# Kernel tuning notes

Measured on AMD Instinct MI355X. Metric: run time of the kernel, lower is better.

## Reference

```python
import jax, jax.numpy as jnp
import numpy as np

NS, NC, T, NB = 32, 16, 64, 512
NSC = NS + NC


def setup_inputs() -> dict:
    key = jax.random.key(0)
    k1, k2, k3, k4, k5 = jax.random.split(key, 5)
    # SPD cost matrices so Quu is invertible (as assumed by the LQR math)
    L = jax.random.normal(k1, (NB, T, NSC, NSC), jnp.float32) * 0.1
    Q = L @ jnp.swapaxes(L, -1, -2) + jnp.eye(NSC, dtype=jnp.float32)
    p = jax.random.normal(k2, (NB, T, NSC), jnp.float32)
    x_init = jax.random.normal(k3, (NB, NS), jnp.float32)
    # stable-ish LTI dynamics
    A = 0.9 * jnp.eye(NS, dtype=jnp.float32) + 0.01 * jax.random.normal(k4, (NS, NS), jnp.float32)
    B = 0.1 * jax.random.normal(k5, (NS, NC), jnp.float32)
    dt = jnp.float32(0.1)
    return {"x_init": x_init, "Q": Q, "p": p, "A": A, "B": B, "dt": dt}


def _lqr(x_init, Q, p, A, B):
    ns, nc = A.shape[0], B.shape[1]
    nb, Th = Q.shape[0], Q.shape[1]
    dtype = Q.dtype

    # --- nominal rollout with zero control: x_{t+1} = A x_t ---
    def roll(x, _):
        return x @ A.T, x
    _, cx = jax.lax.scan(roll, x_init, None, length=Th)   # [T,B,ns] states x_0..x_{T-1}
    cu = jnp.zeros((Th, nb, nc), dtype)                    # current_u = 0
    xu = jnp.concatenate([cx, cu], -1)                     # [T,B,nsc]

    Qs = jnp.swapaxes(Q, 0, 1)                             # [T,B,nsc,nsc]
    ps = jnp.swapaxes(p, 0, 1)                             # [T,B,nsc]
    p_new = jnp.einsum('tbij,tbj->tbi', Qs, xu) + ps       # [T,B,nsc]

    F = jnp.concatenate([A, B], axis=1)                    # [ns, nsc]

    # --- backward Riccati recursion (V=v=0 at t=T-1 makes Qt=Q[T-1]) ---
    def bwd(carry, inp):
        V, v = carry                                       # [B,ns,ns], [B,ns]
        Qt_in, qt_in = inp
        Qt = Qt_in + jnp.einsum('si,bst,tj->bij', F, V, F)
        qt = qt_in + v @ F                                 # F^T v
        Qxx, Qxu = Qt[:, :ns, :ns], Qt[:, :ns, ns:]
        Qux, Quu = Qt[:, ns:, :ns], Qt[:, ns:, ns:]
        qx, qu = qt[:, :ns], qt[:, ns:]
        Quu_inv = jnp.linalg.pinv(Quu)
        Kt = -Quu_inv @ Qux                                # [B,nc,ns]
        kt = -jnp.einsum('bij,bj->bi', Quu_inv, qu)        # [B,nc]
        KtT = jnp.swapaxes(Kt, -1, -2)
        Vn = Qxx + Qxu @ Kt + KtT @ Qux + KtT @ Quu @ Kt
        vn = (qx + jnp.einsum('bij,bj->bi', Qxu, kt)
              + jnp.einsum('bij,bj->bi', KtT, qu)
              + jnp.einsum('bij,bj->bi', KtT @ Quu, kt))
        return (Vn, vn), (Kt, kt)

    V0 = jnp.zeros((nb, ns, ns), dtype)
    v0 = jnp.zeros((nb, ns), dtype)
    _, (Ks, ks) = jax.lax.scan(bwd, (V0, v0), (Qs, p_new), reverse=True)

    # --- forward rollout with feedback policy ---
    def fwd(carry, inp):
        xt, cost = carry
        Kt, kt, cxt, cut, Qt, pt = inp
        dut = jnp.einsum('bij,bj->bi', Kt, xt - cxt) + kt
        ut = dut + cut
        xut = jnp.concatenate([xt, ut], -1)
        cost = cost + 0.5 * jnp.einsum('bi,bij,bj->b', xut, Qt, xut) + (xut * pt).sum(-1)
        xn = xt @ A.T + ut @ B.T
        return (xn, cost), (xt, ut)

    (_, cost), (xs, us) = jax.lax.scan(
        fwd, (x_init, jnp.zeros(nb, dtype)), (Ks, ks, cx, cu, Qs, ps))
    x = jnp.swapaxes(xs, 0, 1)   # [B,T,ns]  (states x_0..x_{T-1}, matching x[...,:-1,:])
    u = jnp.swapaxes(us, 0, 1)   # [B,T,nc]
    return x, u, cost


def reference(x_init, Q, p, A, B, dt):
    # dt only matters for nonlinear relinearization; with constant LTI (A,B) it is unused.
    return _lqr(x_init, Q, p, A, B)
```

## Files before the change

kernel.cpp:

```cpp
#include <hip/hip_runtime.h>


#define NSd 32
#define NCd 16
#define Td 64
#define NBd 512
#define NSCd 48
#define SQS 52
#define TP 40

typedef __bf16 bf16x8 __attribute__((ext_vector_type(8)));
typedef __bf16 bf16x4 __attribute__((ext_vector_type(4)));
typedef float f32x4 __attribute__((ext_vector_type(4)));

#define MFMA16(a, b, c) __builtin_amdgcn_mfma_f32_16x16x32_bf16(a, b, c, 0, 0, 0)

#define XOFF ((size_t)0)
#define UOFF ((size_t)NBd * Td * NSd)
#define COFF (UOFF + (size_t)NBd * Td * NCd)

__device__ __forceinline__ float rdl(float v, int l) {
  return __uint_as_float(__builtin_amdgcn_readlane(__float_as_uint(v), l));
}

__device__ __forceinline__ void bar_lgkm() {
  asm volatile("s_waitcnt lgkmcnt(0)\n\ts_barrier" ::: "memory");
}

union LdsU {
  struct {
    __bf16 FTh[48][TP], FTl[48][TP];
    __bf16 Vh[32][TP], Vl[32][TP];
    __bf16 WTh[48][TP], WTl[48][TP];
    __bf16 Xh[32][TP], Xl[32][TP];
    __bf16 KTh[32][TP], KTl[32][TP];
    float Quu[16][17];
    float qt[48];
    float vv[32];
    float kt[16];
  } bw;
  struct {
    float K2T[2][16 * 36];
    float kv2[2][16];
    float d[32];
    float xs[32];
    float uu[16];
  } fw;
};

#define SQSTORE(i, v)                            \
  do {                                           \
    int _r = (i) / 12, _c = (i) - _r * 12;       \
    *(float4*)&sQ[_r * SQS + _c * 4] = (v);      \
  } while (0)

__global__ __launch_bounds__(256, 2) void lqr_kernel(
    const float* __restrict__ x_init, const float* __restrict__ Qg,
    const float* __restrict__ pg, const float* __restrict__ Ag,
    const float* __restrict__ Bg, float* __restrict__ out,
    float* __restrict__ wsK, float* __restrict__ wskv) {
  const int b = blockIdx.x;
  const int tid = threadIdx.x;
  const int w = tid >> 6;
  const int lane = tid & 63;
  const int fn = lane & 15;
  const int quad = lane >> 4;
  const int k0 = quad * 8;

  __shared__ __attribute__((aligned(16))) float sQ[48 * SQS];
  __shared__ __attribute__((aligned(16))) float scx[Td][NSd];
  __shared__ __attribute__((aligned(16))) float sFf[NSd][SQS];
  __shared__ __attribute__((aligned(16))) LdsU U;
  __shared__ float scostp[4];

  for (int idx = tid; idx < 1536; idx += 256) {
    int i = idx / 48, j = idx - i * 48;
    sFf[i][j] = (j < 32) ? Ag[i * 32 + j] : Bg[i * 16 + (j - 32)];
  }
  for (int idx = tid; idx < 1536; idx += 256) {
    int a = idx >> 5, k = idx & 31;
    float f = (a < 32) ? Ag[k * 32 + a] : Bg[k * 16 + (a - 32)];
    __bf16 h = (__bf16)f;
    U.bw.FTh[a][k] = h;
    U.bw.FTl[a][k] = (__bf16)(f - (float)h);
  }
  for (int idx = tid; idx < 1024; idx += 256) {
    int r = idx >> 5, c = idx & 31;
    __bf16 z = (__bf16)0.f;
    U.bw.Vh[r][c] = z; U.bw.Vl[r][c] = z;
    U.bw.Xh[r][c] = z; U.bw.Xl[r][c] = z;
    U.bw.KTh[r][c] = z; U.bw.KTl[r][c] = z;
  }
  if (tid < 32) {
    scx[0][tid] = x_init[b * 32 + tid];
    U.bw.vv[tid] = 0.f;
  }
  {
    const float4* src = (const float4*)(Qg + ((size_t)b * Td + 63) * 2304);
    float4 v0 = src[tid];
    float4 v1 = src[tid + 256];
    SQSTORE(tid, v0);
    SQSTORE(tid + 256, v1);
    if (tid < 64) {
      float4 v2 = src[tid + 512];
      SQSTORE(tid + 512, v2);
    }
  }
  float ppf = 0.f;
  if (w == 3 && lane < 48) ppf = pg[((size_t)b * Td + 63) * 48 + lane];
  __syncthreads();

  if (w == 0) {
    for (int t2 = 0; t2 < Td - 1; ++t2) {
      if (lane < 32) {
        float acc = 0.f;
#pragma unroll
        for (int j = 0; j < 32; j += 4) {
          float4 a4 = *(const float4*)&sFf[lane][j];
          acc += a4.x * scx[t2][j] + a4.y * scx[t2][j + 1] +
                 a4.z * scx[t2][j + 2] + a4.w * scx[t2][j + 3];
        }
        scx[t2 + 1][lane] = acc;
      }
    }
  }
  __syncthreads();

  float cAcc = 0.f;
  float dAcc = 0.f;

  for (int t = Td - 1; t >= 0; --t) {
    const int sw = 3 - (t & 1);
    float4 pf0, pf1, pf2;
    float ppfn;
    if (t > 0) {
      const float4* src = (const float4*)(Qg + ((size_t)b * Td + (t - 1)) * 2304);
      pf0 = src[tid];
      pf1 = src[tid + 256];
      if (tid < 64) pf2 = src[tid + 512];
      if (w == 3 && lane < 48) ppfn = pg[((size_t)b * Td + t - 1) * 48 + lane];
    }
    if (w < 3) {
      const int I = w;
      bf16x8 aH = *(const bf16x8*)&U.bw.FTh[16 * I + fn][k0];
      bf16x8 aL = *(const bf16x8*)&U.bw.FTl[16 * I + fn][k0];
#pragma unroll
      for (int J = 0; J < 2; ++J) {
        bf16x8 bH = *(const bf16x8*)&U.bw.Vh[16 * J + fn][k0];
        bf16x8 bL = *(const bf16x8*)&U.bw.Vl[16 * J + fn][k0];
        f32x4 acc = {0.f, 0.f, 0.f, 0.f};
        acc = MFMA16(aL, bH, acc);
        acc = MFMA16(aH, bL, acc);
        acc = MFMA16(aH, bH, acc);
#pragma unroll
        for (int r = 0; r < 4; ++r) {
          float v = acc[r];
          __bf16 h = (__bf16)v;
          U.bw.WTh[16 * I + 4 * quad + r][16 * J + fn] = h;
          U.bw.WTl[16 * I + 4 * quad + r][16 * J + fn] = (__bf16)(v - (float)h);
        }
      }
    } else if (lane < 48) {
      float acc1 = ppf;
#pragma unroll
      for (int k = 0; k < 32; ++k) acc1 += sQ[k * SQS + lane] * scx[t][k];
      if (lane < 32) cAcc += 0.5f * scx[t][lane] * (acc1 + ppf);
      float acc = acc1;
#pragma unroll
      for (int k = 0; k < 32; ++k) acc += U.bw.vv[k] * sFf[k][lane];
      U.bw.qt[lane] = acc;
    }
    bar_lgkm();

    f32x4 accQ = {0.f, 0.f, 0.f, 0.f};
    if (w < 2) {
      const int I = w;
      bf16x8 aH = *(const bf16x8*)&U.bw.WTh[16 * I + fn][k0];
      bf16x8 aL = *(const bf16x8*)&U.bw.WTl[16 * I + fn][k0];
      {
        bf16x8 bH = *(const bf16x8*)&U.bw.FTh[16 * I + fn][k0];
        bf16x8 bL = *(const bf16x8*)&U.bw.FTl[16 * I + fn][k0];
#pragma unroll
        for (int r = 0; r < 4; ++r)
          accQ[r] = sQ[(16 * I + 4 * quad + r) * SQS + 16 * I + fn];
        accQ = MFMA16(aL, bH, accQ);
        accQ = MFMA16(aH, bL, accQ);
        accQ = MFMA16(aH, bH, accQ);
      }
      {
        bf16x8 bH = *(const bf16x8*)&U.bw.FTh[32 + fn][k0];
        bf16x8 bL = *(const bf16x8*)&U.bw.FTl[32 + fn][k0];
        f32x4 acc;
#pragma unroll
        for (int r = 0; r < 4; ++r)
          acc[r] = sQ[(16 * I + 4 * quad + r) * SQS + 32 + fn];
        acc = MFMA16(aL, bH, acc);
        acc = MFMA16(aH, bL, acc);
        acc = MFMA16(aH, bH, acc);
#pragma unroll
        for (int r = 0; r < 4; ++r) {
          float v = acc[r];
          __bf16 h = (__bf16)v;
          U.bw.Xh[16 * I + 4 * quad + r][fn] = h;
          U.bw.Xl[16 * I + 4 * quad + r][fn] = (__bf16)(v - (float)h);
        }
      }
    } else if (w == 2) {
      bf16x8 aH = *(const bf16x8*)&U.bw.WTh[fn][k0];
      bf16x8 aL = *(const bf16x8*)&U.bw.WTl[fn][k0];
      bf16x8 bH = *(const bf16x8*)&U.bw.FTh[16 + fn][k0];
      bf16x8 bL = *(const bf16x8*)&U.bw.FTl[16 + fn][k0];
#pragma unroll
      for (int r = 0; r < 4; ++r)
        accQ[r] = sQ[(4 * quad + r) * SQS + 16 + fn];
      accQ = MFMA16(aL, bH, accQ);
      accQ = MFMA16(aH, bL, accQ);
      accQ = MFMA16(aH, bH, accQ);
    } else {
      bf16x8 aH = *(const bf16x8*)&U.bw.WTh[32 + fn][k0];
      bf16x8 aL = *(const bf16x8*)&U.bw.WTl[32 + fn][k0];
      bf16x8 bH = *(const bf16x8*)&U.bw.FTh[32 + fn][k0];
      bf16x8 bL = *(const bf16x8*)&U.bw.FTl[32 + fn][k0];
      f32x4 acc;
#pragma unroll
      for (int r = 0; r < 4; ++r)
        acc[r] = sQ[(32 + 4 * quad + r) * SQS + 32 + fn];
      acc = MFMA16(aL, bH, acc);
      acc = MFMA16(aH, bL, acc);
      acc = MFMA16(aH, bH, acc);
#pragma unroll
      for (int r = 0; r < 4; ++r) U.bw.Quu[4 * quad + r][fn] = acc[r];
    }
    bar_lgkm();

    if (t > 0) {
      SQSTORE(tid, pf0);
      SQSTORE(tid + 256, pf1);
      if (tid < 64) SQSTORE(tid + 512, pf2);
      if (w == 3 && lane < 48) ppf = ppfn;
    }

    if (w == sw) {
      float rhs[16];
      if (lane < 32) {
        bf16x8 xh0 = *(const bf16x8*)&U.bw.Xh[lane][0];
        bf16x8 xh1 = *(const bf16x8*)&U.bw.Xh[lane][8];
        bf16x8 xl0 = *(const bf16x8*)&U.bw.Xl[lane][0];
        bf16x8 xl1 = *(const bf16x8*)&U.bw.Xl[lane][8];
#pragma unroll
        for (int i = 0; i < 8; ++i) {
          rhs[i] = (float)xh0[i] + (float)xl0[i];
          rhs[8 + i] = (float)xh1[i] + (float)xl1[i];
        }
      } else {
#pragma unroll
        for (int i = 0; i < 16; ++i) rhs[i] = U.bw.qt[32 + i];
      }
      float quu[16];
#pragma unroll
      for (int i = 0; i < 16; ++i) quu[i] = U.bw.Quu[i][fn];
#pragma unroll
      for (int r = 0; r < 15; ++r) {
        float inv = __builtin_amdgcn_rcpf(rdl(quu[r], r));
#pragma unroll
        for (int i = r + 1; i < 16; ++i) {
          float m = rdl(quu[i], r) * inv;
          rhs[i] -= m * rhs[r];
          quu[i] -= m * quu[r];
        }
      }
      float xx[16];
#pragma unroll
      for (int r = 15; r >= 0; --r) {
        float s = rhs[r];
#pragma unroll
        for (int c = r + 1; c < 16; ++c) s -= rdl(quu[r], c) * xx[c];
        xx[r] = s * __builtin_amdgcn_rcpf(rdl(quu[r], r));
      }
      if (lane < 32) {
        bf16x8 h0, l0, h1, l1;
#pragma unroll
        for (int u = 0; u < 8; ++u) {
          float kv = -xx[u];
          __bf16 hh = (__bf16)kv;
          h0[u] = hh; l0[u] = (__bf16)(kv - (float)hh);
          float kv2 = -xx[8 + u];
          __bf16 hh2 = (__bf16)kv2;
          h1[u] = hh2; l1[u] = (__bf16)(kv2 - (float)hh2);
        }
        *(bf16x8*)&U.bw.KTh[lane][0] = h0;
        *(bf16x8*)&U.bw.KTh[lane][8] = h1;
        *(bf16x8*)&U.bw.KTl[lane][0] = l0;
        *(bf16x8*)&U.bw.KTl[lane][8] = l1;
        float4* dst = (float4*)(wsK + (((size_t)b * Td + t) * 32 + lane) * 16);
        float4 v0 = {-xx[0], -xx[1], -xx[2], -xx[3]};
        float4 v1 = {-xx[4], -xx[5], -xx[6], -xx[7]};
        float4 v2 = {-xx[8], -xx[9], -xx[10], -xx[11]};
        float4 v3 = {-xx[12], -xx[13], -xx[14], -xx[15]};
        dst[0] = v0; dst[1] = v1; dst[2] = v2; dst[3] = v3;
      } else if (lane == 32) {
#pragma unroll
        for (int u = 0; u < 16; ++u) U.bw.kt[u] = -xx[u];
        float4* dst = (float4*)(wskv + ((size_t)b * Td + t) * 16);
        float4 v0 = {-xx[0], -xx[1], -xx[2], -xx[3]};
        float4 v1 = {-xx[4], -xx[5], -xx[6], -xx[7]};
        float4 v2 = {-xx[8], -xx[9], -xx[10], -xx[11]};
        float4 v3 = {-xx[12], -xx[13], -xx[14], -xx[15]};
        dst[0] = v0; dst[1] = v1; dst[2] = v2; dst[3] = v3;
        float s = 0.f;
#pragma unroll
        for (int i = 0; i < 16; ++i) s += U.bw.qt[32 + i] * xx[i];
        dAcc -= 0.5f * s;
      }
      if (sw == 3) {
        float acc = 0.f;
        bf16x8 xh0, xh1, xl0, xl1;
        if (lane < 32) {
          xh0 = *(const bf16x8*)&U.bw.Xh[lane][0];
          xh1 = *(const bf16x8*)&U.bw.Xh[lane][8];
          xl0 = *(const bf16x8*)&U.bw.Xl[lane][0];
          xl1 = *(const bf16x8*)&U.bw.Xl[lane][8];
          acc = U.bw.qt[lane];
        }
#pragma unroll
        for (int u = 0; u < 8; ++u) {
          float kt0 = -rdl(xx[u], 32);
          float kt1 = -rdl(xx[8 + u], 32);
          if (lane < 32) {
            acc += ((float)xh0[u] + (float)xl0[u]) * kt0;
            acc += ((float)xh1[u] + (float)xl1[u]) * kt1;
          }
        }
        if (lane < 32) U.bw.vv[lane] = acc;
      }
    }
    bar_lgkm();

    if (w == 0) {
      bf16x8 aH = *(const bf16x8*)&U.bw.Xh[fn][k0];
      bf16x8 aL = *(const bf16x8*)&U.bw.Xl[fn][k0];
      bf16x8 bH = *(const bf16x8*)&U.bw.KTh[fn][k0];
      bf16x8 bL = *(const bf16x8*)&U.bw.KTl[fn][k0];
      accQ = MFMA16(aL, bH, accQ);
      accQ = MFMA16(aH, bL, accQ);
      accQ = MFMA16(aH, bH, accQ);
#pragma unroll
      for (int r = 0; r < 4; ++r) {
        float v = accQ[r];
        __bf16 h = (__bf16)v;
        U.bw.Vh[4 * quad + r][fn] = h;
        U.bw.Vl[4 * quad + r][fn] = (__bf16)(v - (float)h);
      }
    } else if (w == 1) {
      bf16x8 aH = *(const bf16x8*)&U.bw.Xh[16 + fn][k0];
      bf16x8 aL = *(const bf16x8*)&U.bw.Xl[16 + fn][k0];
      bf16x8 bH = *(const bf16x8*)&U.bw.KTh[16 + fn][k0];
      bf16x8 bL = *(const bf16x8*)&U.bw.KTl[16 + fn][k0];
      accQ = MFMA16(aL, bH, accQ);
      accQ = MFMA16(aH, bL, accQ);
      accQ = MFMA16(aH, bH, accQ);
#pragma unroll
      for (int r = 0; r < 4; ++r) {
        float v = accQ[r];
        __bf16 h = (__bf16)v;
        U.bw.Vh[16 + 4 * quad + r][16 + fn] = h;
        U.bw.Vl[16 + 4 * quad + r][16 + fn] = (__bf16)(v - (float)h);
      }
    } else if (w == 2) {
      bf16x8 aH = *(const bf16x8*)&U.bw.Xh[fn][k0];
      bf16x8 aL = *(const bf16x8*)&U.bw.Xl[fn][k0];
      bf16x8 bH = *(const bf16x8*)&U.bw.KTh[16 + fn][k0];
      bf16x8 bL = *(const bf16x8*)&U.bw.KTl[16 + fn][k0];
      accQ = MFMA16(aL, bH, accQ);
      accQ = MFMA16(aH, bL, accQ);
      accQ = MFMA16(aH, bH, accQ);
      bf16x4 th, tl;
#pragma unroll
      for (int r = 0; r < 4; ++r) {
        float v = accQ[r];
        __bf16 h = (__bf16)v;
        __bf16 l = (__bf16)(v - (float)h);
        U.bw.Vh[4 * quad + r][16 + fn] = h;
        U.bw.Vl[4 * quad + r][16 + fn] = l;
        th[r] = h; tl[r] = l;
      }
      *(bf16x4*)&U.bw.Vh[16 + fn][4 * quad] = th;
      *(bf16x4*)&U.bw.Vl[16 + fn][4 * quad] = tl;
    } else if (sw == 2) {
      if (lane < 32) {
        bf16x8 xh0 = *(const bf16x8*)&U.bw.Xh[lane][0];
        bf16x8 xh1 = *(const bf16x8*)&U.bw.Xh[lane][8];
        bf16x8 xl0 = *(const bf16x8*)&U.bw.Xl[lane][0];
        bf16x8 xl1 = *(const bf16x8*)&U.bw.Xl[lane][8];
        float acc = U.bw.qt[lane];
#pragma unroll
        for (int u = 0; u < 8; ++u) {
          acc += ((float)xh0[u] + (float)xl0[u]) * U.bw.kt[u];
          acc += ((float)xh1[u] + (float)xl1[u]) * U.bw.kt[8 + u];
        }
        U.bw.vv[lane] = acc;
      }
    }
    bar_lgkm();
  }

  if (w == 3) {
    float rv = (lane < 32) ? cAcc : 0.f;
    rv += __shfl_down(rv, 32);
    rv += __shfl_down(rv, 16);
    rv += __shfl_down(rv, 8);
    rv += __shfl_down(rv, 4);
    rv += __shfl_down(rv, 2);
    rv += __shfl_down(rv, 1);
    if (lane == 0) scostp[0] = rv;
  }
  if (lane == 32 && w >= 2) scostp[w - 1] = dAcc;
  __syncthreads();

  if (w == 0) {
    {
      const float4* src = (const float4*)(wsK + ((size_t)b * Td) * 512);
      float4 ka = src[lane * 2], kb = src[lane * 2 + 1];
      int jj = lane >> 1, ib = (lane & 1) * 8;
      float* kt2 = U.fw.K2T[0];
      kt2[(ib + 0) * 36 + jj] = ka.x; kt2[(ib + 1) * 36 + jj] = ka.y;
      kt2[(ib + 2) * 36 + jj] = ka.z; kt2[(ib + 3) * 36 + jj] = ka.w;
      kt2[(ib + 4) * 36 + jj] = kb.x; kt2[(ib + 5) * 36 + jj] = kb.y;
      kt2[(ib + 6) * 36 + jj] = kb.z; kt2[(ib + 7) * 36 + jj] = kb.w;
      if (lane < 16) U.fw.kv2[0][lane] = wskv[(size_t)b * Td * 16 + lane];
    }
    float xr = (lane < 32) ? scx[0][lane] : 0.f;
    for (int t = 0; t < Td; ++t) {
      const int cur = t & 1, nxt = cur ^ 1;
      float4 pa, pb;
      float pk;
      if (t < Td - 1) {
        const float4* src = (const float4*)(wsK + ((size_t)b * Td + t + 1) * 512);
        pa = src[lane * 2];
        pb = src[lane * 2 + 1];
        if (lane < 16) pk = wskv[((size_t)b * Td + t + 1) * 16 + lane];
      }
      if (lane < 32) {
        U.fw.d[lane] = xr - scx[t][lane];
        U.fw.xs[lane] = xr;
        out[XOFF + ((size_t)b * Td + t) * 32 + lane] = xr;
      }
      if (lane < 16) {
        float uv = U.fw.kv2[cur][lane];
        const float* kr = &U.fw.K2T[cur][lane * 36];
#pragma unroll
        for (int j4 = 0; j4 < 8; ++j4) {
          float4 kk = *(const float4*)&kr[j4 * 4];
          float4 dd = *(const float4*)&U.fw.d[j4 * 4];
          uv += kk.x * dd.x + kk.y * dd.y + kk.z * dd.z + kk.w * dd.w;
        }
        U.fw.uu[lane] = uv;
        out[UOFF + ((size_t)b * Td + t) * 16 + lane] = uv;
      }
      if (lane < 32) {
        float acc = 0.f;
#pragma unroll
        for (int j4 = 0; j4 < 8; ++j4) {
          float4 ff = *(const float4*)&sFf[lane][j4 * 4];
          float4 xv = *(const float4*)&U.fw.xs[j4 * 4];
          acc += ff.x * xv.x + ff.y * xv.y + ff.z * xv.z + ff.w * xv.w;
        }
#pragma unroll
        for (int j4 = 0; j4 < 4; ++j4) {
          float4 ff = *(const float4*)&sFf[lane][32 + j4 * 4];
          float4 uv = *(const float4*)&U.fw.uu[j4 * 4];
          acc += ff.x * uv.x + ff.y * uv.y + ff.z * uv.z + ff.w * uv.w;
        }
        xr = acc;
      }
      if (t < Td - 1) {
        int jj = lane >> 1, ib = (lane & 1) * 8;
        float* kt2 = U.fw.K2T[nxt];
        kt2[(ib + 0) * 36 + jj] = pa.x; kt2[(ib + 1) * 36 + jj] = pa.y;
        kt2[(ib + 2) * 36 + jj] = pa.z; kt2[(ib + 3) * 36 + jj] = pa.w;
        kt2[(ib + 4) * 36 + jj] = pb.x; kt2[(ib + 5) * 36 + jj] = pb.y;
        kt2[(ib + 6) * 36 + jj] = pb.z; kt2[(ib + 7) * 36 + jj] = pb.w;
        if (lane < 16) U.fw.kv2[nxt][lane] = pk;
      }
    }
    if (lane == 0) out[COFF + b] = scostp[0] + scostp[1] + scostp[2];
  }
}

extern "C" void kernel_launch(void* const* d_in, const int* in_sizes, int n_in,
                              void* d_out, int out_size, void* d_ws, size_t ws_size,
                              hipStream_t stream) {
  const float* x_init = (const float*)d_in[0];
  const float* Qg = (const float*)d_in[1];
  const float* pg = (const float*)d_in[2];
  const float* Ag = (const float*)d_in[3];
  const float* Bg = (const float*)d_in[4];
  float* out = (float*)d_out;
  float* wsK = (float*)d_ws;
  float* wskv = wsK + (size_t)NBd * Td * NSd * NCd;
  lqr_kernel<<<NBd, 256, 0, stream>>>(x_init, Qg, pg, Ag, Bg, out, wsK, wskv);
}
```

Before: 663.4 us.

## Restructure backward Riccati step into two barrier phases with fixed wave roles

Each backward step is reorganized so waves 0-2 compute W=F^T V and then the Qt blocks (Qxx pieces, Qxu, Quu) before the first barrier. A single fixed wave 3 then does the Quu solve, the v update and all three V-block MFMAs, instead of alternating solver waves with extra barriers. This removes two of the four block barriers per timestep and the alternating-wave bookkeeping. The cost is serializing more MFMA work onto wave 3 and some extra LDS for the Qd staging. The Q prefetch is also spread over three waves instead of four.

Measured after the change: 636.2 us. 1.04x faster.

```diff
diff --git a/kernel.cpp b/kernel.cpp
--- a/kernel.cpp
+++ b/kernel.cpp
@@ -35,9 +35,9 @@
     __bf16 Xh[32][TP], Xl[32][TP];
     __bf16 KTh[32][TP], KTl[32][TP];
     float Quu[16][17];
+    float Qd[3][16][17];
     float qt[48];
     float vv[32];
-    float kt[16];
   } bw;
   struct {
     float K2T[2][16 * 36];
@@ -130,16 +130,19 @@
   float dAcc = 0.f;
 
   for (int t = Td - 1; t >= 0; --t) {
-    const int sw = 3 - (t & 1);
     float4 pf0, pf1, pf2;
     float ppfn;
     if (t > 0) {
-      const float4* src = (const float4*)(Qg + ((size_t)b * Td + (t - 1)) * 2304);
-      pf0 = src[tid];
-      pf1 = src[tid + 256];
-      if (tid < 64) pf2 = src[tid + 512];
-      if (w == 3 && lane < 48) ppfn = pg[((size_t)b * Td + t - 1) * 48 + lane];
-    }
+      if (w < 3) {
+        const float4* src = (const float4*)(Qg + ((size_t)b * Td + (t - 1)) * 2304);
+        pf0 = src[tid];
+        pf1 = src[tid + 192];
+        pf2 = src[tid + 384];
+      } else if (lane < 48) {
+        ppfn = pg[((size_t)b * Td + t - 1) * 48 + lane];
+      }
+    }
+
     if (w < 3) {
       const int I = w;
       bf16x8 aH = *(const bf16x8*)&U.bw.FTh[16 * I + fn][k0];
@@ -160,6 +163,66 @@
           U.bw.WTl[16 * I + 4 * quad + r][16 * J + fn] = (__bf16)(v - (float)h);
         }
       }
+      bf16x8 wH = *(const bf16x8*)&U.bw.WTh[16 * I + fn][k0];
+      bf16x8 wL = *(const bf16x8*)&U.bw.WTl[16 * I + fn][k0];
+      if (I == 2) {
+        bf16x8 bH = *(const bf16x8*)&U.bw.FTh[32 + fn][k0];
+        bf16x8 bL = *(const bf16x8*)&U.bw.FTl[32 + fn][k0];
+        f32x4 acc;
+#pragma unroll
+        for (int r = 0; r < 4; ++r)
+          acc[r] = sQ[(32 + 4 * quad + r) * SQS + 32 + fn];
+        acc = MFMA16(wL, bH, acc);
+        acc = MFMA16(wH, bL, acc);
+        acc = MFMA16(wH, bH, acc);
+#pragma unroll
+        for (int r = 0; r < 4; ++r) U.bw.Quu[4 * quad + r][fn] = acc[r];
+      } else {
+        {
+          bf16x8 bH = *(const bf16x8*)&U.bw.FTh[16 * I + fn][k0];
+          bf16x8 bL = *(const bf16x8*)&U.bw.FTl[16 * I + fn][k0];
+          f32x4 acc;
+#pragma unroll
+          for (int r = 0; r < 4; ++r)
+            acc[r] = sQ[(16 * I + 4 * quad + r) * SQS + 16 * I + fn];
+          acc = MFMA16(wL, bH, acc);
+          acc = MFMA16(wH, bL, acc);
+          acc = MFMA16(wH, bH, acc);
+#pragma unroll
+          for (int r = 0; r < 4; ++r) U.bw.Qd[I * 2][4 * quad + r][fn] = acc[r];
+        }
+        if (I == 0) {
+          bf16x8 bH = *(const bf16x8*)&U.bw.FTh[16 + fn][k0];
+          bf16x8 bL = *(const bf16x8*)&U.bw.FTl[16 + fn][k0];
+          f32x4 acc;
+#pragma unroll
+          for (int r = 0; r < 4; ++r)
+            acc[r] = sQ[(4 * quad + r) * SQS + 16 + fn];
+          acc = MFMA16(wL, bH, acc);
+          acc = MFMA16(wH, bL, acc);
+          acc = MFMA16(wH, bH, acc);
+#pragma unroll
+          for (int r = 0; r < 4; ++r) U.bw.Qd[1][4 * quad + r][fn] = acc[r];
+        }
+        {
+          bf16x8 bH = *(const bf16x8*)&U.bw.FTh[32 + fn][k0];
+          bf16x8 bL = *(const bf16x8*)&U.bw.FTl[32 + fn][k0];
+          f32x4 acc;
+#pragma unroll
+          for (int r = 0; r < 4; ++r)
+            acc[r] = sQ[(16 * I + 4 * quad + r) * SQS + 32 + fn];
+          acc = MFMA16(wL, bH, acc);
+          acc = MFMA16(wH, bL, acc);
+          acc = MFMA16(wH, bH, acc);
+#pragma unroll
+          for (int r = 0; r < 4; ++r) {
+            float v = acc[r];
+            __bf16 h = (__bf16)v;
+            U.bw.Xh[16 * I + 4 * quad + r][fn] = h;
+            U.bw.Xl[16 * I + 4 * quad + r][fn] = (__bf16)(v - (float)h);
+          }
+        }
+      }
     } else if (lane < 48) {
       float acc1 = ppf;
 #pragma unroll
@@ -172,75 +235,16 @@
     }
     bar_lgkm();
 
-    f32x4 accQ = {0.f, 0.f, 0.f, 0.f};
-    if (w < 2) {
-      const int I = w;
-      bf16x8 aH = *(const bf16x8*)&U.bw.WTh[16 * I + fn][k0];
-      bf16x8 aL = *(const bf16x8*)&U.bw.WTl[16 * I + fn][k0];
-      {
-        bf16x8 bH = *(const bf16x8*)&U.bw.FTh[16 * I + fn][k0];
-        bf16x8 bL = *(const bf16x8*)&U.bw.FTl[16 * I + fn][k0];
-#pragma unroll
-        for (int r = 0; r < 4; ++r)
-          accQ[r] = sQ[(16 * I + 4 * quad + r) * SQS + 16 * I + fn];
-        accQ = MFMA16(aL, bH, accQ);
-        accQ = MFMA16(aH, bL, accQ);
-        accQ = MFMA16(aH, bH, accQ);
-      }
-      {
-        bf16x8 bH = *(const bf16x8*)&U.bw.FTh[32 + fn][k0];
-        bf16x8 bL = *(const bf16x8*)&U.bw.FTl[32 + fn][k0];
-        f32x4 acc;
-#pragma unroll
-        for (int r = 0; r < 4; ++r)
-          acc[r] = sQ[(16 * I + 4 * quad + r) * SQS + 32 + fn];
-        acc = MFMA16(aL, bH, acc);
-        acc = MFMA16(aH, bL, acc);
-        acc = MFMA16(aH, bH, acc);
-#pragma unroll
-        for (int r = 0; r < 4; ++r) {
-          float v = acc[r];
-          __bf16 h = (__bf16)v;
-          U.bw.Xh[16 * I + 4 * quad + r][fn] = h;
-          U.bw.Xl[16 * I + 4 * quad + r][fn] = (__bf16)(v - (float)h);
-        }
-      }
-    } else if (w == 2) {
-      bf16x8 aH = *(const bf16x8*)&U.bw.WTh[fn][k0];
-      bf16x8 aL = *(const bf16x8*)&U.bw.WTl[fn][k0];
-      bf16x8 bH = *(const bf16x8*)&U.bw.FTh[16 + fn][k0];
-      bf16x8 bL = *(const bf16x8*)&U.bw.FTl[16 + fn][k0];
-#pragma unroll
-      for (int r = 0; r < 4; ++r)
-        accQ[r] = sQ[(4 * quad + r) * SQS + 16 + fn];
-      accQ = MFMA16(aL, bH, accQ);
-      accQ = MFMA16(aH, bL, accQ);
-      accQ = MFMA16(aH, bH, accQ);
-    } else {
-      bf16x8 aH = *(const bf16x8*)&U.bw.WTh[32 + fn][k0];
-      bf16x8 aL = *(const bf16x8*)&U.bw.WTl[32 + fn][k0];
-      bf16x8 bH = *(const bf16x8*)&U.bw.FTh[32 + fn][k0];
-      bf16x8 bL = *(const bf16x8*)&U.bw.FTl[32 + fn][k0];
-      f32x4 acc;
-#pragma unroll
-      for (int r = 0; r < 4; ++r)
-        acc[r] = sQ[(32 + 4 * quad + r) * SQS + 32 + fn];
-      acc = MFMA16(aL, bH, acc);
-      acc = MFMA16(aH, bL, acc);
-      acc = MFMA16(aH, bH, acc);
-#pragma unroll
-      for (int r = 0; r < 4; ++r) U.bw.Quu[4 * quad + r][fn] = acc[r];
-    }
-    bar_lgkm();
-
     if (t > 0) {
-      SQSTORE(tid, pf0);
-      SQSTORE(tid + 256, pf1);
-      if (tid < 64) SQSTORE(tid + 512, pf2);
-      if (w == 3 && lane < 48) ppf = ppfn;
-    }
-
-    if (w == sw) {
+      if (w < 3) {
+        SQSTORE(tid, pf0);
+        SQSTORE(tid + 192, pf1);
+        SQSTORE(tid + 384, pf2);
+      } else if (lane < 48) {
+        ppf = ppfn;
+      }
+    }
+    if (w == 3) {
       float rhs[16];
       if (lane < 32) {
         bf16x8 xh0 = *(const bf16x8*)&U.bw.Xh[lane][0];
@@ -299,8 +303,6 @@
         float4 v3 = {-xx[12], -xx[13], -xx[14], -xx[15]};
         dst[0] = v0; dst[1] = v1; dst[2] = v2; dst[3] = v3;
       } else if (lane == 32) {
-#pragma unroll
-        for (int u = 0; u < 16; ++u) U.bw.kt[u] = -xx[u];
         float4* dst = (float4*)(wskv + ((size_t)b * Td + t) * 16);
         float4 v0 = {-xx[0], -xx[1], -xx[2], -xx[3]};
         float4 v1 = {-xx[4], -xx[5], -xx[6], -xx[7]};
@@ -312,7 +314,7 @@
         for (int i = 0; i < 16; ++i) s += U.bw.qt[32 + i] * xx[i];
         dAcc -= 0.5f * s;
       }
-      if (sw == 3) {
+      {
         float acc = 0.f;
         bf16x8 xh0, xh1, xl0, xl1;
         if (lane < 32) {
@@ -333,79 +335,74 @@
         }
         if (lane < 32) U.bw.vv[lane] = acc;
       }
+      {
+        bf16x8 aH = *(const bf16x8*)&U.bw.Xh[fn][k0];
+        bf16x8 aL = *(const bf16x8*)&U.bw.Xl[fn][k0];
+        bf16x8 bH = *(const bf16x8*)&U.bw.KTh[fn][k0];
+        bf16x8 bL = *(const bf16x8*)&U.bw.KTl[fn][k0];
+        f32x4 acc;
+#pragma unroll
+        for (int r = 0; r < 4; ++r) acc[r] = U.bw.Qd[0][4 * quad + r][fn];
+        acc = MFMA16(aL, bH, acc);
+        acc = MFMA16(aH, bL, acc);
+        acc = MFMA16(aH, bH, acc);
+#pragma unroll
+        for (int r = 0; r < 4; ++r) {
+          float v = acc[r];
+          __bf16 h = (__bf16)v;
+          U.bw.Vh[4 * quad + r][fn] = h;
+          U.bw.Vl[4 * quad + r][fn] = (__bf16)(v - (float)h);
+        }
+      }
+      {
+        bf16x8 aH = *(const bf16x8*)&U.bw.Xh[16 + fn][k0];
+        bf16x8 aL = *(const bf16x8*)&U.bw.Xl[16 + fn][k0];
+        bf16x8 bH = *(const bf16x8*)&U.bw.KTh[16 + fn][k0];
+        bf16x8 bL = *(const bf16x8*)&U.bw.KTl[16 + fn][k0];
+        f32x4 acc;
+#pragma unroll
+        for (int r = 0; r < 4; ++r) acc[r] = U.bw.Qd[2][4 * quad + r][fn];
+        acc = MFMA16(aL, bH, acc);
+        acc = MFMA16(aH, bL, acc);
+        acc = MFMA16(aH, bH, acc);
+#pragma unroll
+        for (int r = 0; r < 4; ++r) {
+          float v = acc[r];
+          __bf16 h = (__bf16)v;
+          U.bw.Vh[16 + 4 * quad + r][16 + fn] = h;
+          U.bw.Vl[16 + 4 * quad + r][16 + fn] = (__bf16)(v - (float)h);
+        }
+      }
+      {
+        bf16x8 aH = *(const bf16x8*)&U.bw.Xh[fn][k0];
+        bf16x8 aL = *(const bf16x8*)&U.bw.Xl[fn][k0];
+        bf16x8 bH = *(const bf16x8*)&U.bw.KTh[16 + fn][k0];
+        bf16x8 bL = *(const bf16x8*)&U.bw.KTl[16 + fn][k0];
+        f32x4 acc;
+#pragma unroll
+        for (int r = 0; r < 4; ++r) acc[r] = U.bw.Qd[1][4 * quad + r][fn];
+        acc = MFMA16(aL, bH, acc);
+        acc = MFMA16(aH, bL, acc);
+        acc = MFMA16(aH, bH, acc);
+        bf16x4 th, tl;
+#pragma unroll
+        for (int r = 0; r < 4; ++r) {
+          float v = acc[r];
+          __bf16 h = (__bf16)v;
+          __bf16 l = (__bf16)(v - (float)h);
+          U.bw.Vh[4 * quad + r][16 + fn] = h;
+          U.bw.Vl[4 * quad + r][16 + fn] = l;
+          th[r] = h; tl[r] = l;
+        }
+        *(bf16x4*)&U.bw.Vh[16 + fn][4 * quad] = th;
+        *(bf16x4*)&U.bw.Vl[16 + fn][4 * quad] = tl;
+      }
     }
     bar_lgkm();
-
-    if (w == 0) {
-      bf16x8 aH = *(const bf16x8*)&U.bw.Xh[fn][k0];
-      bf16x8 aL = *(const bf16x8*)&U.bw.Xl[fn][k0];
-      bf16x8 bH = *(const bf16x8*)&U.bw.KTh[fn][k0];
-      bf16x8 bL = *(const bf16x8*)&U.bw.KTl[fn][k0];
-      accQ = MFMA16(aL, bH, accQ);
-      accQ = MFMA16(aH, bL, accQ);
-      accQ = MFMA16(aH, bH, accQ);
-#pragma unroll
-      for (int r = 0; r < 4; ++r) {
-        float v = accQ[r];
-        __bf16 h = (__bf16)v;
-        U.bw.Vh[4 * quad + r][fn] = h;
-        U.bw.Vl[4 * quad + r][fn] = (__bf16)(v - (float)h);
-      }
-    } else if (w == 1) {
-      bf16x8 aH = *(const bf16x8*)&U.bw.Xh[16 + fn][k0];
-      bf16x8 aL = *(const bf16x8*)&U.bw.Xl[16 + fn][k0];
-      bf16x8 bH = *(const bf16x8*)&U.bw.KTh[16 + fn][k0];
-      bf16x8 bL = *(const bf16x8*)&U.bw.KTl[16 + fn][k0];
-      accQ = MFMA16(aL, bH, accQ);
-      accQ = MFMA16(aH, bL, accQ);
-      accQ = MFMA16(aH, bH, accQ);
-#pragma unroll
-      for (int r = 0; r < 4; ++r) {
-        float v = accQ[r];
-        __bf16 h = (__bf16)v;
-        U.bw.Vh[16 + 4 * quad + r][16 + fn] = h;
-        U.bw.Vl[16 + 4 * quad + r][16 + fn] = (__bf16)(v - (float)h);
-      }
-    } else if (w == 2) {
-      bf16x8 aH = *(const bf16x8*)&U.bw.Xh[fn][k0];
-      bf16x8 aL = *(const bf16x8*)&U.bw.Xl[fn][k0];
-      bf16x8 bH = *(const bf16x8*)&U.bw.KTh[16 + fn][k0];
-      bf16x8 bL = *(const bf16x8*)&U.bw.KTl[16 + fn][k0];
-      accQ = MFMA16(aL, bH, accQ);
-      accQ = MFMA16(aH, bL, accQ);
-      accQ = MFMA16(aH, bH, accQ);
-      bf16x4 th, tl;
-#pragma unroll
-      for (int r = 0; r < 4; ++r) {
-        float v = accQ[r];
-        __bf16 h = (__bf16)v;
-        __bf16 l = (__bf16)(v - (float)h);
-        U.bw.Vh[4 * quad + r][16 + fn] = h;
-        U.bw.Vl[4 * quad + r][16 + fn] = l;
-        th[r] = h; tl[r] = l;
-      }
-      *(bf16x4*)&U.bw.Vh[16 + fn][4 * quad] = th;
-      *(bf16x4*)&U.bw.Vl[16 + fn][4 * quad] = tl;
-    } else if (sw == 2) {
-      if (lane < 32) {
-        bf16x8 xh0 = *(const bf16x8*)&U.bw.Xh[lane][0];
-        bf16x8 xh1 = *(const bf16x8*)&U.bw.Xh[lane][8];
-        bf16x8 xl0 = *(const bf16x8*)&U.bw.Xl[lane][0];
-        bf16x8 xl1 = *(const bf16x8*)&U.bw.Xl[lane][8];
-        float acc = U.bw.qt[lane];
-#pragma unroll
-        for (int u = 0; u < 8; ++u) {
-          acc += ((float)xh0[u] + (float)xl0[u]) * U.bw.kt[u];
-          acc += ((float)xh1[u] + (float)xl1[u]) * U.bw.kt[8 + u];
-        }
-        U.bw.vv[lane] = acc;
-      }
-    }
-    bar_lgkm();
   }
 
   if (w == 3) {
-    float rv = (lane < 32) ? cAcc : 0.f;
+    float rv = (lane < 32) ? cAcc : (lane == 32 ? dAcc : 0.f);
     rv += __shfl_down(rv, 32);
     rv += __shfl_down(rv, 16);
     rv += __shfl_down(rv, 8);
@@ -414,7 +411,6 @@
     rv += __shfl_down(rv, 1);
     if (lane == 0) scostp[0] = rv;
   }
-  if (lane == 32 && w >= 2) scostp[w - 1] = dAcc;
   __syncthreads();
 
   if (w == 0) {
@@ -483,7 +479,7 @@
         if (lane < 16) U.fw.kv2[nxt][lane] = pk;
       }
     }
-    if (lane == 0) out[COFF + b] = scostp[0] + scostp[1] + scostp[2];
+    if (lane == 0) out[COFF + b] = scostp[0];
   }
 }
 
```
